# Kernel optimization log

Hardware: AMD Instinct MI355X
Metric: run time of the kernel (lower is better)

## Reference

```python
import jax, jax.numpy as jnp
import numpy as np

TAU = 1.0
LOSS_WEIGHT = 1.0
N = 4_000_000


def setup_inputs() -> dict:
    key = jax.random.key(0)
    k1, k2 = jax.random.split(key)

    def make_boxes(k):
        u = jax.random.uniform(k, (N, 5), dtype=jnp.float32)
        xy = u[:, :2] * 1024.0                 # centers in a 1024px image
        wh = u[:, 2:4] * 100.0 + 4.0           # box sizes in [4, 104)
        r = (u[:, 4:5] - 0.5) * jnp.pi         # angle in [-pi/2, pi/2)
        return jnp.concatenate([xy, wh, r], axis=-1)

    return {"pred": make_boxes(k1), "target": make_boxes(k2)}


def xy_wh_r_2_xy_sigma(xywhr):
    """(N,5) rbox -> (mu (N,2), sigma (N,2,2)) via R @ (S/2)^2 @ R^T closed form."""
    xy = xywhr[..., :2]
    wh = jnp.clip(xywhr[..., 2:4], 1e-7, 1e7)
    r = xywhr[..., 4]
    c, s = jnp.cos(r), jnp.sin(r)
    a = (0.5 * wh[..., 0]) ** 2  # (w/2)^2
    b = (0.5 * wh[..., 1]) ** 2  # (h/2)^2
    s00 = a * c * c + b * s * s
    s11 = a * s * s + b * c * c
    s01 = (a - b) * s * c
    sigma = jnp.stack(
        [jnp.stack([s00, s01], -1), jnp.stack([s01, s11], -1)], -2
    )  # (N,2,2)
    return xy, sigma


def _det2(m):
    return m[..., 0, 0] * m[..., 1, 1] - m[..., 0, 1] * m[..., 1, 0]


def _inv2(m):
    det = _det2(m)
    adj = jnp.stack(
        [jnp.stack([m[..., 1, 1], -m[..., 0, 1]], -1),
         jnp.stack([-m[..., 1, 0], m[..., 0, 0]], -1)], -2)
    return adj / det[..., None, None]


def kld_loss(mu_p, sigma_p, mu_t, sigma_t, tau):
    delta = mu_p - mu_t                                # (N,2)
    sigma_t_inv = _inv2(sigma_t)                       # (N,2,2)
    # delta^T Sigma_t^{-1} delta
    term1 = jnp.einsum('ni,nij,nj->n', delta, sigma_t_inv, delta)
    # tr(Sigma_t^{-1} Sigma_p) + log(det Sigma_t / det Sigma_p)
    tr = jnp.einsum('nij,nji->n', sigma_t_inv, sigma_p)
    term2 = tr + jnp.log(_det2(sigma_t) / _det2(sigma_p))
    dis = term1 + term2 - 2.0
    kl_dis = jnp.maximum(dis, 1e-6)
    # fun == 'log1p'
    loss = 1.0 - 1.0 / (tau + jnp.log1p(kl_dis))
    return loss[:, None]                               # (N,1) like torch version


def reference(pred, target):
    mu_p, sigma_p = xy_wh_r_2_xy_sigma(pred)
    mu_t, sigma_t = xy_wh_r_2_xy_sigma(target)
    return kld_loss(mu_p, sigma_p, mu_t, sigma_t, TAU) * LOSS_WEIGHT
```

## Files before the change

kernel.cpp:

```cpp
#include <hip/hip_runtime.h>
#include <math.h>
#include <stdint.h>

#ifndef TAU_CONST
#define TAU_CONST 1.0f
#endif


__device__ __forceinline__ void rbox_to_gauss(float x, float y, float w, float h, float r,
                                              float& mx, float& my,
                                              float& s00, float& s01, float& s11, float& det) {
    w = fminf(fmaxf(w, 1e-7f), 1e7f);
    h = fminf(fmaxf(h, 1e-7f), 1e7f);
    float a = 0.25f * w * w;
    float b = 0.25f * h * h;
    float s2, c2;
    __sincosf(r + r, &s2, &c2);
    float hs = 0.5f * (a + b);
    float hd = 0.5f * (a - b);
    s00 = fmaf(hd, c2, hs);
    s11 = fmaf(-hd, c2, hs);
    s01 = hd * s2;
    det = a * b;
    mx = x; my = y;
}

__device__ __forceinline__ float kld_row(const float* p, const float* t) {
    float pmx, pmy, p00, p01, p11, dp;
    float tmx, tmy, t00, t01, t11, dt;
    rbox_to_gauss(p[0], p[1], p[2], p[3], p[4], pmx, pmy, p00, p01, p11, dp);
    rbox_to_gauss(t[0], t[1], t[2], t[3], t[4], tmx, tmy, t00, t01, t11, dt);
    float dx = pmx - tmx, dy = pmy - tmy;
    float inv_dt = __builtin_amdgcn_rcpf(dt);
    float inv_dp = __builtin_amdgcn_rcpf(dp);
    float term1 = (dx * dx * t11 - 2.0f * dx * dy * t01 + dy * dy * t00) * inv_dt;
    float tr = (t11 * p00 + t00 * p11 - 2.0f * t01 * p01) * inv_dt;
    float term2 = tr + __logf(dt * inv_dp);
    float dis = term1 + term2 - 2.0f;
    float kl = fmaxf(dis, 1e-6f);
    float l1p = __logf(1.0f + kl);
    return 1.0f - __builtin_amdgcn_rcpf(TAU_CONST + l1p);
}


__device__ __forceinline__ void gload_lds16(const void* g, void* l) {
    __builtin_amdgcn_global_load_lds((const __attribute__((address_space(1))) uint32_t*)g,
                                     (__attribute__((address_space(3))) uint32_t*)l,
                                     16, 0, 0);
}

__global__ void __launch_bounds__(256, 8) gdloss_lds_kernel(const float* __restrict__ pred,
                                                            const float* __restrict__ target,
                                                            float* __restrict__ out) {
    __shared__ float lds[5120];
    const int tid = threadIdx.x;
    const int wv  = tid >> 6;
    const int ln  = tid & 63;
    const long long base = (long long)blockIdx.x * 2560;

#pragma unroll
    for (int k = 0; k < 5; ++k) {
        int c = wv * 5 + k;
        const float* g = (c < 10) ? (pred   + base + c * 256 + ln * 4)
                                  : (target + base + (c - 10) * 256 + ln * 4);
        gload_lds16(g, &lds[c * 256]);
    }
    __syncthreads();

    const float2* lp = (const float2*)&lds[10 * tid];
    const float2* lt = (const float2*)&lds[2560 + 10 * tid];
    float2 p0 = lp[0], p1 = lp[1], p2 = lp[2], p3 = lp[3], p4 = lp[4];
    float2 t0 = lt[0], t1 = lt[1], t2 = lt[2], t3 = lt[3], t4 = lt[4];

    float pr0[5] = {p0.x, p0.y, p1.x, p1.y, p2.x};
    float pr1[5] = {p2.y, p3.x, p3.y, p4.x, p4.y};
    float tr0[5] = {t0.x, t0.y, t1.x, t1.y, t2.x};
    float tr1[5] = {t2.y, t3.x, t3.y, t4.x, t4.y};

    float2 o;
    o.x = kld_row(pr0, tr0);
    o.y = kld_row(pr1, tr1);
    ((float2*)out)[(size_t)blockIdx.x * 256 + tid] = o;
}

__global__ void gdloss_tail_kernel(const float* __restrict__ pred,
                                   const float* __restrict__ target,
                                   float* __restrict__ out, int start, int n) {
    int i = start + blockIdx.x * blockDim.x + threadIdx.x;
    if (i >= n) return;
    float p[5], t[5];
#pragma unroll
    for (int k = 0; k < 5; ++k) {
        p[k] = pred[5 * i + k];
        t[k] = target[5 * i + k];
    }
    out[i] = kld_row(p, t);
}

extern "C" void kernel_launch(void* const* d_in, const int* in_sizes, int n_in,
                              void* d_out, int out_size, void* d_ws, size_t ws_size,
                              hipStream_t stream) {
    const float* pred   = (const float*)d_in[0];
    const float* target = (const float*)d_in[1];
    float* out = (float*)d_out;
    int n  = in_sizes[0] / 5;
    int nb = n / 512;
    if (nb > 0) {
        gdloss_lds_kernel<<<nb, 256, 0, stream>>>(pred, target, out);
    }
    int start = nb * 512;
    int rem = n - start;
    if (rem > 0) {
        int tb = (rem + 255) / 256;
        gdloss_tail_kernel<<<tb, 256, 0, stream>>>(pred, target, out, start, n);
    }
}
```

Measured before the change: 178.5 us.

## Convert to persistent grid-stride kernel with double-buffered LDS prefetch

Replaces the one-shot per-block kernel with a persistent kernel capped at 2048 blocks. Each block walks 256-row tiles in grid-stride order and prefetches the next tile into a second LDS buffer with async global-to-LDS loads while it computes the current one. The intent is to overlap memory transfer with compute and to cut block launch and scheduling overhead. In exchange each thread now handles one row per tile instead of two and writes scalar stores, and fewer bytes are in flight per block than with a large oversubscribed grid.

```diff
diff --git a/kernel.cpp b/kernel.cpp
--- a/kernel.cpp
+++ b/kernel.cpp
@@ -49,38 +49,49 @@
                                      16, 0, 0);
 }
 
-__global__ void __launch_bounds__(256, 8) gdloss_lds_kernel(const float* __restrict__ pred,
-                                                            const float* __restrict__ target,
-                                                            float* __restrict__ out) {
-    __shared__ float lds[5120];
+#define ROWS_PER_TILE 256
+#define FLOATS_PER_TILE (ROWS_PER_TILE * 5)
+
+__global__ void __launch_bounds__(256, 8)
+gdloss_pipe_kernel(const float* __restrict__ pred,
+                   const float* __restrict__ target,
+                   float* __restrict__ out, int ntiles) {
+    __shared__ float lds[2][2 * FLOATS_PER_TILE];
     const int tid = threadIdx.x;
     const int wv  = tid >> 6;
     const int ln  = tid & 63;
-    const long long base = (long long)blockIdx.x * 2560;
+    const int stride = gridDim.x;
 
+    int t = blockIdx.x;
+    if (t < ntiles) {
+        for (int c = wv; c < 10; c += 4) {
+            const float* g = (c < 5)
+                ? (pred   + (long long)t * FLOATS_PER_TILE + c * 256 + ln * 4)
+                : (target + (long long)t * FLOATS_PER_TILE + (c - 5) * 256 + ln * 4);
+            gload_lds16(g, &lds[0][c * 256]);
+        }
+    }
+
+    int buf = 0;
+    for (; t < ntiles; t += stride) {
+        __syncthreads();
+        int tn = t + stride;
+        if (tn < ntiles) {
+            for (int c = wv; c < 10; c += 4) {
+                const float* g = (c < 5)
+                    ? (pred   + (long long)tn * FLOATS_PER_TILE + c * 256 + ln * 4)
+                    : (target + (long long)tn * FLOATS_PER_TILE + (c - 5) * 256 + ln * 4);
+                gload_lds16(g, &lds[buf ^ 1][c * 256]);
+            }
+        }
+        const float* lp = &lds[buf][5 * tid];
+        const float* lt = &lds[buf][FLOATS_PER_TILE + 5 * tid];
+        float p[5], tt[5];
 #pragma unroll
-    for (int k = 0; k < 5; ++k) {
-        int c = wv * 5 + k;
-        const float* g = (c < 10) ? (pred   + base + c * 256 + ln * 4)
-                                  : (target + base + (c - 10) * 256 + ln * 4);
-        gload_lds16(g, &lds[c * 256]);
+        for (int k = 0; k < 5; ++k) { p[k] = lp[k]; tt[k] = lt[k]; }
+        out[(long long)t * ROWS_PER_TILE + tid] = kld_row(p, tt);
+        buf ^= 1;
     }
-    __syncthreads();
-
-    const float2* lp = (const float2*)&lds[10 * tid];
-    const float2* lt = (const float2*)&lds[2560 + 10 * tid];
-    float2 p0 = lp[0], p1 = lp[1], p2 = lp[2], p3 = lp[3], p4 = lp[4];
-    float2 t0 = lt[0], t1 = lt[1], t2 = lt[2], t3 = lt[3], t4 = lt[4];
-
-    float pr0[5] = {p0.x, p0.y, p1.x, p1.y, p2.x};
-    float pr1[5] = {p2.y, p3.x, p3.y, p4.x, p4.y};
-    float tr0[5] = {t0.x, t0.y, t1.x, t1.y, t2.x};
-    float tr1[5] = {t2.y, t3.x, t3.y, t4.x, t4.y};
-
-    float2 o;
-    o.x = kld_row(pr0, tr0);
-    o.y = kld_row(pr1, tr1);
-    ((float2*)out)[(size_t)blockIdx.x * 256 + tid] = o;
 }
 
 __global__ void gdloss_tail_kernel(const float* __restrict__ pred,
@@ -103,12 +114,13 @@
     const float* pred   = (const float*)d_in[0];
     const float* target = (const float*)d_in[1];
     float* out = (float*)d_out;
-    int n  = in_sizes[0] / 5;
-    int nb = n / 512;
-    if (nb > 0) {
-        gdloss_lds_kernel<<<nb, 256, 0, stream>>>(pred, target, out);
+    int n      = in_sizes[0] / 5;
+    int ntiles = n / ROWS_PER_TILE;
+    if (ntiles > 0) {
+        int blocks = ntiles < 2048 ? ntiles : 2048;
+        gdloss_pipe_kernel<<<blocks, 256, 0, stream>>>(pred, target, out, ntiles);
     }
-    int start = nb * 512;
+    int start = ntiles * ROWS_PER_TILE;
     int rem = n - start;
     if (rem > 0) {
         int tb = (rem + 255) / 256;
```

Measured after the change: 180.4 us. Within noise of the previous version (+1.1%).
